# Kernel optimization log

Hardware: AMD Instinct MI355X
Metric: run time of the kernel (lower is better)

The kernel has to match this reference:

```python
import jax, jax.numpy as jnp
import numpy as np

DIM = 1024
NUM_HEADS = 16
HEAD_DIM = DIM // NUM_HEADS
TAU = 1.0
LAMBDA_JUMP = 0.6
LAMBDA_LOCAL = 0.4
MIN_ENTROPY = 0.5
WINDOW = 3
EPS = 1e-10


def local_diffusion_kernel(seq_len, strength, window=WINDOW):
    # Banded Gaussian kernel, row-normalized. [S, S]
    i = jnp.arange(seq_len)
    d = i[:, None] - i[None, :]
    k = jnp.where(jnp.abs(d) <= window,
                  jnp.exp(-(d.astype(jnp.float32) ** 2) / (2.0 * strength ** 2)),
                  0.0)
    return k / (k.sum(axis=-1, keepdims=True) + EPS)


def setup_inputs() -> dict:
    key = jax.random.key(0)
    ks = jax.random.split(key, 9)
    scale = 0.02
    x = jax.random.normal(ks[0], (2, 2048, DIM), dtype=jnp.float32)
    Wq = jax.random.normal(ks[1], (DIM, DIM), dtype=jnp.float32) * scale
    bq = jax.random.normal(ks[2], (DIM,), dtype=jnp.float32) * scale
    Wk = jax.random.normal(ks[3], (DIM, DIM), dtype=jnp.float32) * scale
    bk = jax.random.normal(ks[4], (DIM,), dtype=jnp.float32) * scale
    Wv = jax.random.normal(ks[5], (DIM, DIM), dtype=jnp.float32) * scale
    bv = jax.random.normal(ks[6], (DIM,), dtype=jnp.float32) * scale
    Wo = jax.random.normal(ks[7], (DIM, DIM), dtype=jnp.float32) * scale
    bo = jax.random.normal(ks[8], (DIM,), dtype=jnp.float32) * scale
    return {"x": x, "Wq": Wq, "bq": bq, "Wk": Wk, "bk": bk,
            "Wv": Wv, "bv": bv, "Wo": Wo, "bo": bo}


def reference(x, Wq, bq, Wk, bk, Wv, bv, Wo, bo):
    B, S, D = x.shape
    H, hd = NUM_HEADS, HEAD_DIM
    # torch Linear: y = x @ W.T + b
    Q = (x @ Wq.T + bq).reshape(B, S, H, hd).transpose(0, 2, 1, 3)  # [B,H,S,hd]
    K = (x @ Wk.T + bk).reshape(B, S, H, hd).transpose(0, 2, 1, 3)
    V = (x @ Wv.T + bv).reshape(B, S, H, hd).transpose(0, 2, 1, 3)

    scores = jnp.einsum('bhqd,bhkd->bhqk', Q, K) / (TAU * np.sqrt(hd).astype(np.float32))
    A = jax.nn.softmax(scores, axis=-1)  # [B,H,S,S]

    # Per-row entropy gating (detach-based in torch: forward value is unchanged)
    entropy = -jnp.sum(A * jnp.log(A + EPS), axis=-1, keepdims=True)
    stable = jax.lax.stop_gradient((entropy >= MIN_ENTROPY).astype(A.dtype))
    A = stable * A + (1.0 - stable) * jax.lax.stop_gradient(A)

    L = local_diffusion_kernel(S, LAMBDA_LOCAL)  # [S,S]
    A_stable = LAMBDA_JUMP * A + (1.0 - LAMBDA_JUMP) * L[None, None, :, :]

    out = jnp.einsum('bhqk,bhkd->bhqd', A_stable, V)  # [B,H,S,hd]
    out = out.transpose(0, 2, 1, 3).reshape(B, S, D)
    return out @ Wo.T + bo
```

## Files before the change

### kernel.cpp

```cpp
#include <hip/hip_runtime.h>
#include <math.h>

typedef __bf16 bf16x8 __attribute__((ext_vector_type(8)));
typedef float f32x4 __attribute__((ext_vector_type(4)));

namespace {
constexpr int DIMC = 1024, NH = 16, HD = 64, SEQ = 2048;
constexpr float SCL2 = 0.1803368801f;
}

__device__ __forceinline__ unsigned short f2b(float f) {
  unsigned u = __float_as_uint(f);
  return (unsigned short)((u + 0x7fffu + ((u >> 16) & 1u)) >> 16);
}
__device__ __forceinline__ float b2f(unsigned short s) {
  return __uint_as_float((unsigned)s << 16);
}
__device__ __forceinline__ unsigned cvtpk(float lo, float hi) {
  unsigned r;
  asm("v_cvt_pk_bf16_f32 %0, %1, %2" : "=v"(r) : "v"(lo), "v"(hi));
  return r;
}
__device__ __forceinline__ void gld16(void* l, const void* g) {
  __builtin_amdgcn_global_load_lds(
      (const __attribute__((address_space(1))) void*)g,
      (__attribute__((address_space(3))) void*)l, 16, 0, 0);
}

__global__ __launch_bounds__(256)
void cvt_all(const float* __restrict__ x,
             const float* __restrict__ w0, const float* __restrict__ w1,
             const float* __restrict__ w2, const float* __restrict__ w3,
             unsigned short* __restrict__ xb, unsigned short* __restrict__ wb) {
  const int bid = blockIdx.x;
  const float* src;
  unsigned short* dst;
  int i;
  if (bid < 2048) {
    src = x; dst = xb; i = bid * 256 + threadIdx.x;
  } else {
    const int r = (bid - 2048) >> 9, lb = (bid - 2048) & 511;
    src = r == 0 ? w0 : r == 1 ? w1 : r == 2 ? w2 : w3;
    dst = wb + (size_t)r * 1048576;
    i = lb * 256 + threadIdx.x;
  }
  const float4* in4 = (const float4*)src;
  float4 a = in4[2 * i], b = in4[2 * i + 1];
  union { unsigned short u[8]; uint4 v; } r;
  r.u[0] = f2b(a.x); r.u[1] = f2b(a.y); r.u[2] = f2b(a.z); r.u[3] = f2b(a.w);
  r.u[4] = f2b(b.x); r.u[5] = f2b(b.y); r.u[6] = f2b(b.z); r.u[7] = f2b(b.w);
  ((uint4*)dst)[i] = r.v;
}

template<int MODE>
__device__ __forceinline__
void gemm_tile128(const unsigned short* __restrict__ A, const unsigned short* __restrict__ W,
                  const float* __restrict__ bias, void* __restrict__ Cout,
                  int bm, int bn, float scl, bool kswz, char* As, char* Bs) {
  const int tid = threadIdx.x, lane = tid & 63, w = tid >> 6;
  const int p = lane & 15, g = lane >> 4;
  const int wr = w >> 1, wc = w & 1;
  const int sr = tid >> 2, sc = (tid & 3) * 8;

  f32x4 acc[4][4];
#pragma unroll
  for (int mf = 0; mf < 4; ++mf)
#pragma unroll
    for (int nf = 0; nf < 4; ++nf)
      acc[mf][nf] = (f32x4){0.f, 0.f, 0.f, 0.f};

  const size_t arow0 = (size_t)(bm + sr) * DIMC + sc;
  const size_t arow1 = (size_t)(bm + 64 + sr) * DIMC + sc;
  const size_t brow0 = (size_t)(bn + sr) * DIMC + sc;
  const size_t brow1 = (size_t)(bn + 64 + sr) * DIMC + sc;

  for (int k0 = 0; k0 < DIMC; k0 += 32) {
    __syncthreads();
    gld16(&As[tid * 16],        &A[arow0 + k0]);
    gld16(&As[4096 + tid * 16], &A[arow1 + k0]);
    gld16(&Bs[tid * 16],        &W[brow0 + k0]);
    gld16(&Bs[4096 + tid * 16], &W[brow1 + k0]);
    __syncthreads();
    bf16x8 af[4], bfr[4];
#pragma unroll
    for (int mf = 0; mf < 4; ++mf)
      af[mf] = *(const bf16x8*)&As[(wr * 64 + mf * 16 + p) * 64 + g * 16];
#pragma unroll
    for (int nf = 0; nf < 4; ++nf)
      bfr[nf] = *(const bf16x8*)&Bs[(wc * 64 + nf * 16 + p) * 64 + g * 16];
#pragma unroll
    for (int mf = 0; mf < 4; ++mf)
#pragma unroll
      for (int nf = 0; nf < 4; ++nf)
        acc[mf][nf] = __builtin_amdgcn_mfma_f32_16x16x32_bf16(af[mf], bfr[nf], acc[mf][nf], 0, 0, 0);
  }

#pragma unroll
  for (int nf = 0; nf < 4; ++nf) {
    const int cg = bn + wc * 64 + nf * 16 + p;
    const float bv = bias[cg & (DIMC - 1)];
#pragma unroll
    for (int mf = 0; mf < 4; ++mf) {
#pragma unroll
      for (int j = 0; j < 4; ++j) {
        const int rg = bm + wr * 64 + mf * 16 + g * 4 + j;
        const float v = (acc[mf][nf][j] + bv) * scl;
        if (MODE == 0) {
          ((float*)Cout)[(size_t)rg * DIMC + cg] = v;
        } else {
          const int bb = rg >> 11, ss = rg & (SEQ - 1);
          const int hh = cg >> 6;
          int dd = cg & (HD - 1);
          if (kswz) dd ^= (ss & 7) << 3;
          ((unsigned short*)Cout)[(((size_t)(bb * NH + hh) * SEQ + ss) * HD) + dd] = f2b(v);
        }
      }
    }
  }
}

__global__ __launch_bounds__(256, 2)
void gemm_qkv(const unsigned short* __restrict__ A, const unsigned short* __restrict__ Wall,
              const float* __restrict__ bq, const float* __restrict__ bk,
              const float* __restrict__ bv, unsigned short* __restrict__ Out) {
  __shared__ char As[8192];
  __shared__ char Bs[8192];
  const int which = blockIdx.z;
  const unsigned short* W = Wall + (size_t)which * 1048576;
  const float* bias = which == 0 ? bq : which == 1 ? bk : bv;
  unsigned short* Cout = Out + (size_t)which * 4194304;
  const float scl = which == 0 ? SCL2 : 1.0f;
  gemm_tile128<1>(A, W, bias, Cout, blockIdx.x * 128, blockIdx.y * 128, scl, which == 1, As, Bs);
}

__global__ __launch_bounds__(256, 2)
void gemm_out(const unsigned short* __restrict__ A, const unsigned short* __restrict__ W,
              const float* __restrict__ bias, float* __restrict__ Cout) {
  __shared__ char As[8192];
  __shared__ char Bs[4096];
  const int tid = threadIdx.x, lane = tid & 63, w = tid >> 6;
  const int p = lane & 15, g = lane >> 4;
  const int wr = w >> 1, wc = w & 1;
  const int bm = blockIdx.x * 128, bn = blockIdx.y * 64;
  const int sr = tid >> 2, sc = (tid & 3) * 8;

  f32x4 acc[4][2];
#pragma unroll
  for (int mf = 0; mf < 4; ++mf)
#pragma unroll
    for (int nf = 0; nf < 2; ++nf)
      acc[mf][nf] = (f32x4){0.f, 0.f, 0.f, 0.f};

  const size_t arow0 = (size_t)(bm + sr) * DIMC + sc;
  const size_t arow1 = (size_t)(bm + 64 + sr) * DIMC + sc;
  const size_t brow  = (size_t)(bn + sr) * DIMC + sc;

  for (int k0 = 0; k0 < DIMC; k0 += 32) {
    __syncthreads();
    gld16(&As[tid * 16],        &A[arow0 + k0]);
    gld16(&As[4096 + tid * 16], &A[arow1 + k0]);
    gld16(&Bs[tid * 16],        &W[brow + k0]);
    __syncthreads();
    bf16x8 af[4], bfr[2];
#pragma unroll
    for (int mf = 0; mf < 4; ++mf)
      af[mf] = *(const bf16x8*)&As[(wr * 64 + mf * 16 + p) * 64 + g * 16];
#pragma unroll
    for (int nf = 0; nf < 2; ++nf)
      bfr[nf] = *(const bf16x8*)&Bs[(wc * 32 + nf * 16 + p) * 64 + g * 16];
#pragma unroll
    for (int mf = 0; mf < 4; ++mf)
#pragma unroll
      for (int nf = 0; nf < 2; ++nf)
        acc[mf][nf] = __builtin_amdgcn_mfma_f32_16x16x32_bf16(af[mf], bfr[nf], acc[mf][nf], 0, 0, 0);
  }

#pragma unroll
  for (int nf = 0; nf < 2; ++nf) {
    const int cg = bn + wc * 32 + nf * 16 + p;
    const float bv = bias[cg];
#pragma unroll
    for (int mf = 0; mf < 4; ++mf) {
#pragma unroll
      for (int j = 0; j < 4; ++j) {
        const int rg = bm + wr * 64 + mf * 16 + g * 4 + j;
        Cout[(size_t)rg * DIMC + cg] = acc[mf][nf][j] + bv;
      }
    }
  }
}

__global__ __launch_bounds__(512, 4)
void attn_fused(const unsigned short* __restrict__ Q, const unsigned short* __restrict__ K,
                const unsigned short* __restrict__ V, unsigned short* __restrict__ Y) {
  __shared__ char Kl[2][8192];
  __shared__ char Vt[2][8192];
  __shared__ char Pl[2][16384];
  const int tid = threadIdx.x, lane = tid & 63, w = tid >> 6;
  const int p = lane & 15, g = lane >> 4;
  const int bh = blockIdx.x, b = bh >> 4, h = bh & 15;
  const int q0 = blockIdx.y * 128;
  const int qwv = q0 + w * 16;
  const size_t base = (size_t)bh * SEQ * HD;
  const unsigned short* Qp = Q + base;
  const unsigned short* Vp = V + base;

  union Vu { bf16x8 v; unsigned short u[8]; };

  bf16x8 qf[2];
#pragma unroll
  for (int ks = 0; ks < 2; ++ks)
    qf[ks] = *(const bf16x8*)&Qp[(size_t)(qwv + p) * HD + ks * 32 + g * 8];

  bf16x8 ones8;
  {
    union { unsigned short u[8]; bf16x8 v; } o;
#pragma unroll
    for (int e = 0; e < 8; ++e) o.u[e] = (p == 0) ? (unsigned short)0x3F80 : (unsigned short)0;
    ones8 = o.v;
  }

  const unsigned short* kSrc = K + base + (size_t)(tid >> 3) * HD + (tid & 7) * 8;
  const int kp = tid & 31, vd0 = ((tid >> 5) & 7) * 8;
  const bool vload = tid < 256;
  const unsigned short* vSrc = Vp + (size_t)(2 * kp) * HD + vd0;

  const int swz = (p & 7) << 4;
  int sCol[2], pwCol[4], colE[8];
#pragma unroll
  for (int ks = 0; ks < 2; ++ks) sCol[ks] = (ks * 64 + g * 16) ^ swz;
#pragma unroll
  for (int nf = 0; nf < 4; ++nf) pwCol[nf] = (nf * 32 + g * 8) ^ swz;
#pragma unroll
  for (int e = 0; e < 8; ++e) colE[e] = (kp * 4) ^ (e << 4);

  f32x4 o2[4];
  f32x4 ol;
#pragma unroll
  for (int nf = 0; nf < 4; ++nf) o2[nf] = (f32x4){0.f, 0.f, 0.f, 0.f};
  ol = (f32x4){0.f, 0.f, 0.f, 0.f};

  Vu v0A, v1A, v0B, v1B;

  auto gldK = [&](int par, int kb) {
    gld16(&Kl[par][tid * 16], kSrc + (size_t)kb * HD);
  };
  auto loadV = [&](Vu& a0, Vu& a1, int kb) {
    if (vload) {
      a0.v = *(const bf16x8*)(vSrc + (size_t)kb * HD);
      a1.v = *(const bf16x8*)(vSrc + (size_t)(kb + 1) * HD);
    }
  };
  auto writeV = [&](int par, Vu& a0, Vu& a1) {
    if (vload) {
      char* vtp = &Vt[par][0] + vd0 * 128;
#pragma unroll
      for (int e = 0; e < 8; ++e) {
        const unsigned val = (unsigned)a0.u[e] | ((unsigned)a1.u[e] << 16);
        *(unsigned*)(vtp + e * 128 + colE[e]) = val;
      }
    }
  };
  auto qkt_sm_stage = [&](int kpar, int ppar) {
    const char* klp = &Kl[kpar][0] + p * 128;
    bf16x8 kf[4][2];
#pragma unroll
    for (int nf = 0; nf < 4; ++nf)
#pragma unroll
      for (int ks = 0; ks < 2; ++ks)
        kf[nf][ks] = *(const bf16x8*)(klp + nf * 2048 + sCol[ks]);
    f32x4 s[4];
#pragma unroll
    for (int nf = 0; nf < 4; ++nf) s[nf] = (f32x4){0.f, 0.f, 0.f, 0.f};
    __builtin_amdgcn_s_setprio(1);
#pragma unroll
    for (int nf = 0; nf < 4; ++nf)
#pragma unroll
      for (int ks = 0; ks < 2; ++ks)
        s[nf] = __builtin_amdgcn_mfma_f32_16x16x32_bf16(kf[nf][ks], qf[ks], s[nf], 0, 0, 0);
    __builtin_amdgcn_s_setprio(0);
#pragma unroll
    for (int nf = 0; nf < 4; ++nf)
#pragma unroll
      for (int j = 0; j < 4; ++j)
        s[nf][j] = exp2f(s[nf][j]);
    char* plp = &Pl[ppar][0] + w * 2048 + p * 128;
#pragma unroll
    for (int nf = 0; nf < 4; ++nf) {
      uint2 val;
      val.x = cvtpk(s[nf][0], s[nf][1]);
      val.y = cvtpk(s[nf][2], s[nf][3]);
      *(uint2*)(plp + pwCol[nf]) = val;
    }
  };
  auto pv = [&](int vpar, int ppar) {
    const char* plp = &Pl[ppar][0] + w * 2048 + p * 128;
    bf16x8 pf[2];
#pragma unroll
    for (int ks = 0; ks < 2; ++ks)
      pf[ks] = *(const bf16x8*)(plp + sCol[ks]);
    const char* vtp = &Vt[vpar][0] + p * 128;
    bf16x8 vb[4][2];
#pragma unroll
    for (int nfd = 0; nfd < 4; ++nfd)
#pragma unroll
      for (int ks = 0; ks < 2; ++ks)
        vb[nfd][ks] = *(const bf16x8*)(vtp + nfd * 2048 + sCol[ks]);
    __builtin_amdgcn_s_setprio(1);
#pragma unroll
    for (int nfd = 0; nfd < 4; ++nfd)
#pragma unroll
      for (int ks = 0; ks < 2; ++ks)
        o2[nfd] = __builtin_amdgcn_mfma_f32_16x16x32_bf16(vb[nfd][ks], pf[ks], o2[nfd], 0, 0, 0);
#pragma unroll
    for (int ks = 0; ks < 2; ++ks)
      ol = __builtin_amdgcn_mfma_f32_16x16x32_bf16(ones8, pf[ks], ol, 0, 0, 0);
    __builtin_amdgcn_s_setprio(0);
  };

  gldK(0, 0);
  loadV(v0A, v1A, 0);
  __syncthreads();
  gldK(1, 64);
  loadV(v0B, v1B, 64);
  qkt_sm_stage(0, 0);
  writeV(0, v0A, v1A);
  __syncthreads();

  for (int it = 0; it < 15; ++it) {
    const int t = 2 * it + 1;
    gldK(0, (t + 1) * 64);
    loadV(v0A, v1A, (t + 1) * 64);
    qkt_sm_stage(1, 1);
    pv(0, 0);
    writeV(1, v0B, v1B);
    __syncthreads();
    gldK(1, (t + 2) * 64);
    loadV(v0B, v1B, (t + 2) * 64);
    qkt_sm_stage(0, 0);
    pv(1, 1);
    writeV(0, v0A, v1A);
    __syncthreads();
  }
  qkt_sm_stage(1, 1);
  pv(0, 0);
  writeV(1, v0B, v1B);
  __syncthreads();
  pv(1, 1);

  const float e1 = 4.3936934e-2f, e2 = 3.7266532e-6f, e3 = 6.1019804e-13f;
  const float lwv[4] = {1.f, e1, e2, e3};
  {
    const int q = qwv + p;
    const float lq = __shfl(ol[0], p);
    const float inv = 0.6f / lq;
    float wsum = 0.f;
#pragma unroll
    for (int dd = -3; dd <= 3; ++dd) {
      const int kk = q + dd;
      if (kk >= 0 && kk < SEQ) wsum += lwv[dd < 0 ? -dd : dd];
    }
    const float wn = 0.4f / (wsum + 1e-10f);
#pragma unroll
    for (int nfd = 0; nfd < 4; ++nfd) {
      const int d0 = nfd * 16 + g * 4;
      float loc[4] = {0.f, 0.f, 0.f, 0.f};
#pragma unroll
      for (int dd = -3; dd <= 3; ++dd) {
        const int kk = q + dd;
        if (kk >= 0 && kk < SEQ) {
          const uint2 lv = *(const uint2*)&Vp[(size_t)kk * HD + d0];
          const float wt = lwv[dd < 0 ? -dd : dd];
          loc[0] = fmaf(wt, b2f((unsigned short)lv.x), loc[0]);
          loc[1] = fmaf(wt, b2f((unsigned short)(lv.x >> 16)), loc[1]);
          loc[2] = fmaf(wt, b2f((unsigned short)lv.y), loc[2]);
          loc[3] = fmaf(wt, b2f((unsigned short)(lv.y >> 16)), loc[3]);
        }
      }
      uint2 st;
      st.x = cvtpk(o2[nfd][0] * inv + loc[0] * wn, o2[nfd][1] * inv + loc[1] * wn);
      st.y = cvtpk(o2[nfd][2] * inv + loc[2] * wn, o2[nfd][3] * inv + loc[3] * wn);
      *(uint2*)&Y[((size_t)(b * SEQ + q)) * DIMC + h * HD + d0] = st;
    }
  }
}

extern "C" void kernel_launch(void* const* d_in, const int* in_sizes, int n_in,
                              void* d_out, int out_size, void* d_ws, size_t ws_size,
                              hipStream_t stream) {
  (void)in_sizes; (void)n_in; (void)out_size; (void)ws_size;
  const float* x  = (const float*)d_in[0];
  const float* Wq = (const float*)d_in[1];
  const float* bq = (const float*)d_in[2];
  const float* Wk = (const float*)d_in[3];
  const float* bk = (const float*)d_in[4];
  const float* Wv = (const float*)d_in[5];
  const float* bv = (const float*)d_in[6];
  const float* Wo = (const float*)d_in[7];
  const float* bo = (const float*)d_in[8];

  char* ws = (char*)d_ws;
  unsigned short* xb  = (unsigned short*)(ws);
  unsigned short* Wqb = (unsigned short*)(ws + 8388608);
  unsigned short* Wob = (unsigned short*)(ws + 14680064);
  unsigned short* Qh  = (unsigned short*)(ws + 16777216);
  unsigned short* Kh  = (unsigned short*)(ws + 25165824);
  unsigned short* Vh  = (unsigned short*)(ws + 33554432);
  unsigned short* Yb  = (unsigned short*)(ws + 41943040);

  dim3 blk(256);
  cvt_all<<<4096, blk, 0, stream>>>(x, Wq, Wk, Wv, Wo, xb, Wqb);

  gemm_qkv<<<dim3(32, 8, 3), blk, 0, stream>>>(xb, Wqb, bq, bk, bv, Qh);

  attn_fused<<<dim3(32, 16), dim3(512), 0, stream>>>(Qh, Kh, Vh, Yb);

  gemm_out<<<dim3(32, 16), blk, 0, stream>>>(Yb, Wob, bo, (float*)d_out);
}
```

Measured before the change: 129.0 us.

## Triple-buffer K tiles and restructure attention pipeline with one barrier per tile

Restructures the attention main loop to use three K LDS buffers loaded two tiles ahead and a single P buffer. Each tile now does QK^T/exp, writes V and P, hits one barrier, then runs PV, instead of overlapping QK^T of one tile with PV of the previous. A custom barrier waits only on outstanding vector-memory loads beyond the most recent ones (vmcnt(3)), so prefetches can stay in flight across it. The aim is deeper prefetch and lower LDS use. The cost is that the hand-tuned waitcnt must be correct, and QK and PV of the same tile are now serialized.

Result: no change. 127.0 us, median of 2 (-1.6%).

```diff
diff --git a/kernel.cpp b/kernel.cpp
--- a/kernel.cpp
+++ b/kernel.cpp
@@ -26,6 +26,11 @@
       (const __attribute__((address_space(1))) void*)g,
       (__attribute__((address_space(3))) void*)l, 16, 0, 0);
 }
+
+#define TBAR() do {                                                        \
+  asm volatile("s_waitcnt vmcnt(3) lgkmcnt(0)\n\ts_barrier" ::: "memory"); \
+  __builtin_amdgcn_sched_barrier(0);                                       \
+} while (0)
 
 __global__ __launch_bounds__(256)
 void cvt_all(const float* __restrict__ x,
@@ -193,9 +198,9 @@
 __global__ __launch_bounds__(512, 4)
 void attn_fused(const unsigned short* __restrict__ Q, const unsigned short* __restrict__ K,
                 const unsigned short* __restrict__ V, unsigned short* __restrict__ Y) {
-  __shared__ char Kl[2][8192];
+  __shared__ char Kl[3][8192];
   __shared__ char Vt[2][8192];
-  __shared__ char Pl[2][16384];
+  __shared__ char Pl[16384];
   const int tid = threadIdx.x, lane = tid & 63, w = tid >> 6;
   const int p = lane & 15, g = lane >> 4;
   const int bh = blockIdx.x, b = bh >> 4, h = bh & 15;
@@ -261,7 +266,7 @@
       }
     }
   };
-  auto qkt_sm_stage = [&](int kpar, int ppar) {
+  auto qkt_sm_stage = [&](int kpar) {
     const char* klp = &Kl[kpar][0] + p * 128;
     bf16x8 kf[4][2];
 #pragma unroll
@@ -284,7 +289,7 @@
 #pragma unroll
       for (int j = 0; j < 4; ++j)
         s[nf][j] = exp2f(s[nf][j]);
-    char* plp = &Pl[ppar][0] + w * 2048 + p * 128;
+    char* plp = &Pl[0] + w * 2048 + p * 128;
 #pragma unroll
     for (int nf = 0; nf < 4; ++nf) {
       uint2 val;
@@ -293,8 +298,8 @@
       *(uint2*)(plp + pwCol[nf]) = val;
     }
   };
-  auto pv = [&](int vpar, int ppar) {
-    const char* plp = &Pl[ppar][0] + w * 2048 + p * 128;
+  auto pv = [&](int vpar) {
+    const char* plp = &Pl[0] + w * 2048 + p * 128;
     bf16x8 pf[2];
 #pragma unroll
     for (int ks = 0; ks < 2; ++ks)
@@ -319,34 +324,33 @@
   };
 
   gldK(0, 0);
+  gldK(1, 64);
   loadV(v0A, v1A, 0);
   __syncthreads();
-  gldK(1, 64);
-  loadV(v0B, v1B, 64);
-  qkt_sm_stage(0, 0);
-  writeV(0, v0A, v1A);
-  __syncthreads();
-
-  for (int it = 0; it < 15; ++it) {
-    const int t = 2 * it + 1;
-    gldK(0, (t + 1) * 64);
-    loadV(v0A, v1A, (t + 1) * 64);
-    qkt_sm_stage(1, 1);
-    pv(0, 0);
-    writeV(1, v0B, v1B);
-    __syncthreads();
-    gldK(1, (t + 2) * 64);
-    loadV(v0B, v1B, (t + 2) * 64);
-    qkt_sm_stage(0, 0);
-    pv(1, 1);
-    writeV(0, v0A, v1A);
-    __syncthreads();
-  }
-  qkt_sm_stage(1, 1);
-  pv(0, 0);
-  writeV(1, v0B, v1B);
-  __syncthreads();
-  pv(1, 1);
+
+  for (int it = 0; it < 5; ++it) {
+    const int t0 = it * 6;
+    gldK(2, (t0 + 2) * 64); loadV(v0B, v1B, (t0 + 1) * 64);
+    qkt_sm_stage(0); writeV(0, v0A, v1A); TBAR(); pv(0);
+
+    gldK(0, (t0 + 3) * 64); loadV(v0A, v1A, (t0 + 2) * 64);
+    qkt_sm_stage(1); writeV(1, v0B, v1B); TBAR(); pv(1);
+
+    gldK(1, (t0 + 4) * 64); loadV(v0B, v1B, (t0 + 3) * 64);
+    qkt_sm_stage(2); writeV(0, v0A, v1A); TBAR(); pv(0);
+
+    gldK(2, (t0 + 5) * 64); loadV(v0A, v1A, (t0 + 4) * 64);
+    qkt_sm_stage(0); writeV(1, v0B, v1B); TBAR(); pv(1);
+
+    gldK(0, (t0 + 6) * 64); loadV(v0B, v1B, (t0 + 5) * 64);
+    qkt_sm_stage(1); writeV(0, v0A, v1A); TBAR(); pv(0);
+
+    gldK(1, (t0 + 7) * 64); loadV(v0A, v1A, (t0 + 6) * 64);
+    qkt_sm_stage(2); writeV(1, v0B, v1B); TBAR(); pv(1);
+  }
+  loadV(v0B, v1B, 31 * 64);
+  qkt_sm_stage(0); writeV(0, v0A, v1A); TBAR(); pv(0);
+  qkt_sm_stage(1); writeV(1, v0B, v1B); TBAR(); pv(1);
 
   const float e1 = 4.3936934e-2f, e2 = 3.7266532e-6f, e3 = 6.1019804e-13f;
   const float lwv[4] = {1.f, e1, e2, e3};
```
